# Optimization experiments

Hardware: AMD Instinct MI355X
Metric: run time of the kernel (lower is better)

Reference implementation:

```python
import jax, jax.numpy as jnp
import numpy as np

B, S, D, H = 2, 2048, 1024, 16
HD = D // H  # head_dim = 64


def setup_inputs() -> dict:
    key = jax.random.key(0)
    ks = jax.random.split(key, 11)
    sc = 1.0 / np.sqrt(D)
    inp = {
        "query": jax.random.normal(ks[0], (B, S, D), jnp.float32),
        "key_": jax.random.normal(ks[1], (B, S, D), jnp.float32),
        "value": jax.random.normal(ks[2], (B, S, D), jnp.float32),
        "Wq": jax.random.normal(ks[3], (D, D), jnp.float32) * sc,
        "bq": jnp.zeros((D,), jnp.float32),
        "Wk": jax.random.normal(ks[4], (D, D), jnp.float32) * sc,
        "bk": jnp.zeros((D,), jnp.float32),
        "Wv": jax.random.normal(ks[5], (D, D), jnp.float32) * sc,
        "bv": jnp.zeros((D,), jnp.float32),
        "Wo": jax.random.normal(ks[6], (D, D), jnp.float32) * sc,
        "bo": jnp.zeros((D,), jnp.float32),
    }
    return inp


def _split_heads(x):
    # [B,S,D] -> [B,H,S,HD]
    return x.reshape(B, -1, H, HD).transpose(0, 2, 1, 3)


def reference(query, key_, value, Wq, bq, Wk, bk, Wv, bv, Wo, bo):
    q = _split_heads(query @ Wq.T + bq)
    k = _split_heads(key_ @ Wk.T + bk)
    v = _split_heads(value @ Wv.T + bv)
    scores = jnp.einsum("bhqd,bhkd->bhqk", q, k) / jnp.sqrt(jnp.float32(HD))
    attn = jax.nn.softmax(scores, axis=-1)  # dropout is identity in eval
    out = jnp.einsum("bhqk,bhkd->bhqd", attn, v)
    out = out.transpose(0, 2, 1, 3).reshape(B, -1, D)
    return out @ Wo.T + bo
```

## Files before the change

### kernel.cpp

```cpp
#include <hip/hip_runtime.h>
#include <hip/hip_bf16.h>
#include <stdint.h>

#define B_  2
#define S_  2048
#define D_  1024
#define H_  16
#define HD_ 64
#define M_  (B_*S_)

typedef __bf16 bf16x8 __attribute__((ext_vector_type(8)));
typedef float  f32x4  __attribute__((ext_vector_type(4)));
typedef unsigned int u32x4 __attribute__((ext_vector_type(4)));
typedef unsigned int u32x2 __attribute__((ext_vector_type(2)));
typedef unsigned short ushort_t;
typedef ushort_t u16x8 __attribute__((ext_vector_type(8)));

#define LOG2E 1.44269504088896f

#if __has_builtin(__builtin_amdgcn_exp2f)
#define EXP2(x) __builtin_amdgcn_exp2f(x)
#else
#define EXP2(x) exp2f(x)
#endif

__device__ __forceinline__ ushort_t f2bf(float f) {
    return __builtin_bit_cast(ushort_t, (__bf16)f);
}
__device__ __forceinline__ bf16x8 load_frag(const ushort_t* p) {
    u32x4 r = *reinterpret_cast<const u32x4*>(p);
    return __builtin_bit_cast(bf16x8, r);
}
__device__ __forceinline__ bf16x8 lds_frag(const ushort_t* p) {
    u32x4 r = *reinterpret_cast<const u32x4*>(p);
    return __builtin_bit_cast(bf16x8, r);
}
__device__ __forceinline__ void gld_lds16(const ushort_t* g, ushort_t* l) {
    __builtin_amdgcn_global_load_lds(
        (const __attribute__((address_space(1))) void*)g,
        (__attribute__((address_space(3))) void*)l, 16, 0, 0);
}

__device__ __forceinline__ void cvt_body(const float* __restrict__ in,
                                         ushort_t* __restrict__ out, int i) {
    f32x4 v0 = *reinterpret_cast<const f32x4*>(in + i);
    f32x4 v1 = *reinterpret_cast<const f32x4*>(in + i + 4);
    u16x8 o;
#pragma unroll
    for (int j = 0; j < 4; ++j) { o[j] = f2bf(v0[j]); o[4 + j] = f2bf(v1[j]); }
    *reinterpret_cast<u16x8*>(out + i) = o;
}

__global__ __launch_bounds__(256) void cvt_all_kernel(
    const float* q, const float* k, const float* v,
    const float* fwq, const float* fwk, const float* fwv, const float* fwo,
    ushort_t* oq, ushort_t* ok, ushort_t* ov,
    ushort_t* owq, ushort_t* owk, ushort_t* owv, ushort_t* owo)
{
    const size_t T = (size_t)M_ * D_;
    const size_t U = (size_t)D_ * D_;
    const size_t idx = ((size_t)blockIdx.x * 256 + threadIdx.x) * 8;
    const float* in; ushort_t* out; size_t off;
    if (idx < 3 * T) {
        const size_t w = idx >> 22; off = idx & (T - 1);
        in  = (w == 0) ? q  : (w == 1) ? k  : v;
        out = (w == 0) ? oq : (w == 1) ? ok : ov;
    } else {
        const size_t r = idx - 3 * T;
        const size_t w = r >> 20; off = r & (U - 1);
        in  = (w == 0) ? fwq : (w == 1) ? fwk : (w == 2) ? fwv : fwo;
        out = (w == 0) ? owq : (w == 1) ? owk : (w == 2) ? owv : owo;
    }
    cvt_body(in, out, (int)off);
}

__device__ __forceinline__ void gemm_body(const ushort_t* __restrict__ X,
                                          const ushort_t* __restrict__ W,
                                          const float* __restrict__ bias,
                                          void* __restrict__ out, int mode)
{
    __shared__ ushort_t lA[2][128 * 32];
    __shared__ ushort_t lB[2][128 * 32];

    const int tid  = threadIdx.x;
    const int lane = tid & 63;
    const int wv   = tid >> 6;
    const int m0   = blockIdx.x * 128;
    const int n0   = blockIdx.y * 128;
    const int wr   = (wv >> 1) * 64;
    const int wc   = (wv & 1) * 64;
    const int l15  = lane & 15;
    const int lg   = lane >> 4;

    f32x4 acc[4][4];
#pragma unroll
    for (int i = 0; i < 4; ++i)
#pragma unroll
        for (int j = 0; j < 4; ++j) acc[i][j] = (f32x4){0.f, 0.f, 0.f, 0.f};

    const int srow = lane >> 2;
    const int sk   = (lane & 3) * 8;
    const int c0   = wv * 2, c1 = wv * 2 + 1;
    const size_t arow0 = (size_t)(m0 + c0 * 16 + srow) * D_ + sk;
    const size_t arow1 = (size_t)(m0 + c1 * 16 + srow) * D_ + sk;
    const size_t brow0 = (size_t)(n0 + c0 * 16 + srow) * D_ + sk;
    const size_t brow1 = (size_t)(n0 + c1 * 16 + srow) * D_ + sk;

    gld_lds16(X + arow0, &lA[0][c0 * 512]);
    gld_lds16(X + arow1, &lA[0][c1 * 512]);
    gld_lds16(W + brow0, &lB[0][c0 * 512]);
    gld_lds16(W + brow1, &lB[0][c1 * 512]);

    const int NKT = D_ / 32;
    for (int kt = 0; kt < NKT; ++kt) {
        const int cur = kt & 1;
        __builtin_amdgcn_s_barrier();
        if (kt + 1 < NKT) {
            const int k0 = (kt + 1) * 32;
            gld_lds16(X + arow0 + k0, &lA[cur ^ 1][c0 * 512]);
            gld_lds16(X + arow1 + k0, &lA[cur ^ 1][c1 * 512]);
            gld_lds16(W + brow0 + k0, &lB[cur ^ 1][c0 * 512]);
            gld_lds16(W + brow1 + k0, &lB[cur ^ 1][c1 * 512]);
            asm volatile("s_waitcnt vmcnt(4)" ::: "memory");
        } else {
            asm volatile("s_waitcnt vmcnt(0)" ::: "memory");
        }
        __builtin_amdgcn_s_barrier();

        bf16x8 a[4], b[4];
#pragma unroll
        for (int i = 0; i < 4; ++i)
            a[i] = lds_frag(&lA[cur][(wr + i * 16 + l15) * 32 + lg * 8]);
#pragma unroll
        for (int j = 0; j < 4; ++j)
            b[j] = lds_frag(&lB[cur][(wc + j * 16 + l15) * 32 + lg * 8]);
#pragma unroll
        for (int i = 0; i < 4; ++i)
#pragma unroll
            for (int j = 0; j < 4; ++j)
                acc[i][j] = __builtin_amdgcn_mfma_f32_16x16x32_bf16(a[i], b[j], acc[i][j], 0, 0, 0);
    }

#pragma unroll
    for (int i = 0; i < 4; ++i) {
#pragma unroll
        for (int j = 0; j < 4; ++j) {
            const int gcol = n0 + wc + j * 16 + l15;
            const float bv = bias[gcol];
#pragma unroll
            for (int r = 0; r < 4; ++r) {
                const int grow = m0 + wr + i * 16 + lg * 4 + r;
                float v = acc[i][j][r] + bv;
                if (mode == 0) v *= 0.125f * LOG2E;
                if (mode == 3) {
                    ((float*)out)[(size_t)grow * D_ + gcol] = v;
                } else {
                    const int b = grow >> 11, s = grow & (S_ - 1);
                    const int h = gcol >> 6,  hd = gcol & 63;
                    size_t addr;
                    if (mode == 2) addr = ((size_t)(b * H_ + h) * HD_ + hd) * S_ + s;
                    else           addr = ((size_t)(b * H_ + h) * S_ + s) * HD_ + hd;
                    ((ushort_t*)out)[addr] = f2bf(v);
                }
            }
        }
    }
}

__global__ __launch_bounds__(256) void qkv_kernel(
    const ushort_t* q_in, const ushort_t* k_in, const ushort_t* v_in,
    const ushort_t* Wq, const ushort_t* Wk, const ushort_t* Wv,
    const float* bq, const float* bk, const float* bv,
    ushort_t* qo, ushort_t* ko, ushort_t* vo)
{
    const int z = blockIdx.z;
    const ushort_t* X  = (z == 0) ? q_in : (z == 1) ? k_in : v_in;
    const ushort_t* W  = (z == 0) ? Wq   : (z == 1) ? Wk   : Wv;
    const float*    bs = (z == 0) ? bq   : (z == 1) ? bk   : bv;
    ushort_t*       o  = (z == 0) ? qo   : (z == 1) ? ko   : vo;
    gemm_body(X, W, bs, o, (z == 2) ? 2 : z);
}

__global__ __launch_bounds__(256) void oproj_kernel(
    const ushort_t* X, const ushort_t* W, const float* bias, float* out)
{
    gemm_body(X, W, bias, out, 3);
}

#define PSTRIDE 72
#define KVB 64
#define NT  (S_ / KVB)
#define AW  8

__global__ __launch_bounds__(512, 4) void attn_kernel(
    const ushort_t* __restrict__ Q, const ushort_t* __restrict__ K,
    const ushort_t* __restrict__ VT, ushort_t* __restrict__ O)
{
    __shared__ ushort_t kbuf[2][KVB * 64];
    __shared__ ushort_t vbuf[2][KVB * 64];
    __shared__ ushort_t plds[AW * 16 * PSTRIDE];

    const int lane  = threadIdx.x & 63;
    const int wv    = threadIdx.x >> 6;
    const int bh    = blockIdx.x;
    const int qb    = blockIdx.y;
    const int qbase = qb * (16 * AW) + wv * 16;
    const int l15   = lane & 15;
    const int lg    = lane >> 4;

    const ushort_t* Qp = Q  + (size_t)bh * S_ * HD_;
    const ushort_t* Kp = K  + (size_t)bh * S_ * HD_;
    const ushort_t* Vp = VT + (size_t)bh * HD_ * S_;

    const int st_id   = threadIdx.x & 255;
    const bool st_k   = (threadIdx.x < 256);
    const ushort_t* Sg = st_k ? Kp : Vp;
    const int gstride  = st_k ? HD_ : S_;
    const int gtile    = st_k ? (KVB * HD_) : KVB;

    const int sm0   = st_id;
    const int srow0 = sm0 >> 3;
    const int scb0  = ((sm0 & 7) ^ (srow0 & 7)) * 8;
    const int sm1   = 256 + st_id;
    const int srow1 = sm1 >> 3;
    const int scb1  = ((sm1 & 7) ^ (srow1 & 7)) * 8;

    int off[4][2];
#pragma unroll
    for (int x = 0; x < 4; ++x)
#pragma unroll
        for (int c = 0; c < 2; ++c)
            off[x][c] = (x * 16 + l15) * 64 + ((c * 32 + lg * 8) ^ ((l15 & 7) << 3));

    bf16x8 aq[2];
#pragma unroll
    for (int c = 0; c < 2; ++c)
        aq[c] = load_frag(Qp + (size_t)(qbase + l15) * HD_ + c * 32 + lg * 8);

    f32x4 accO[4];
#pragma unroll
    for (int dt = 0; dt < 4; ++dt) accO[dt] = (f32x4){0.f, 0.f, 0.f, 0.f};
    float lrun = 0.f;

    ushort_t* pbuf = &plds[wv * 16 * PSTRIDE];

    {
        ushort_t* dst = st_k ? kbuf[0] : vbuf[0];
        gld_lds16(Sg + (size_t)srow0 * gstride + scb0, dst + sm0 * 8);
        gld_lds16(Sg + (size_t)srow1 * gstride + scb1, dst + sm1 * 8);
    }

    for (int t = 0; t < NT; ++t) {
        const int cur = t & 1;
        const ushort_t* kb = kbuf[cur];
        const ushort_t* vb = vbuf[cur];

        __builtin_amdgcn_s_barrier();
        if (t + 1 < NT) {
            const ushort_t* g = Sg + (size_t)(t + 1) * gtile;
            ushort_t* dst = st_k ? kbuf[cur ^ 1] : vbuf[cur ^ 1];
            gld_lds16(g + (size_t)srow0 * gstride + scb0, dst + sm0 * 8);
            gld_lds16(g + (size_t)srow1 * gstride + scb1, dst + sm1 * 8);
            asm volatile("s_waitcnt vmcnt(2)" ::: "memory");
        } else {
            asm volatile("s_waitcnt vmcnt(0)" ::: "memory");
        }
        __builtin_amdgcn_s_barrier();

        f32x4 st[4];
#pragma unroll
        for (int j = 0; j < 4; ++j) st[j] = (f32x4){0.f, 0.f, 0.f, 0.f};
        __builtin_amdgcn_s_setprio(1);
#pragma unroll
        for (int j = 0; j < 4; ++j)
#pragma unroll
            for (int c = 0; c < 2; ++c)
                st[j] = __builtin_amdgcn_mfma_f32_16x16x32_bf16(
                    lds_frag(&kb[off[j][c]]), aq[c], st[j], 0, 0, 0);
        __builtin_amdgcn_s_setprio(0);

        float p[4][4];
#pragma unroll
        for (int j = 0; j < 4; ++j)
#pragma unroll
            for (int r = 0; r < 4; ++r)
                p[j][r] = EXP2(st[j][r]);

#pragma unroll
        for (int j = 0; j < 4; ++j) {
            u32x2 w;
            w[0] = (unsigned)f2bf(p[j][0]) | ((unsigned)f2bf(p[j][1]) << 16);
            w[1] = (unsigned)f2bf(p[j][2]) | ((unsigned)f2bf(p[j][3]) << 16);
            *reinterpret_cast<u32x2*>(&pbuf[l15 * PSTRIDE + j * 16 + lg * 4]) = w;
        }

        float s0 = (p[0][0] + p[0][1]) + (p[0][2] + p[0][3]);
        float s1 = (p[1][0] + p[1][1]) + (p[1][2] + p[1][3]);
        float s2 = (p[2][0] + p[2][1]) + (p[2][2] + p[2][3]);
        float s3 = (p[3][0] + p[3][1]) + (p[3][2] + p[3][3]);
        lrun += (s0 + s1) + (s2 + s3);

        bf16x8 ap[2];
#pragma unroll
        for (int c = 0; c < 2; ++c)
            ap[c] = lds_frag(&pbuf[l15 * PSTRIDE + c * 32 + lg * 8]);

        __builtin_amdgcn_s_setprio(1);
#pragma unroll
        for (int dt = 0; dt < 4; ++dt)
#pragma unroll
            for (int c = 0; c < 2; ++c)
                accO[dt] = __builtin_amdgcn_mfma_f32_16x16x32_bf16(
                    lds_frag(&vb[off[dt][c]]), ap[c], accO[dt], 0, 0, 0);
        __builtin_amdgcn_s_setprio(0);
    }

    lrun += __shfl_xor(lrun, 16);
    lrun += __shfl_xor(lrun, 32);
    const float inv = 1.0f / lrun;
    const int b = bh >> 4, h = bh & 15;
    const size_t rowbase = (size_t)(b * S_ + qbase + l15) * D_ + h * 64;
#pragma unroll
    for (int dt = 0; dt < 4; ++dt) {
        u32x2 w;
        w[0] = (unsigned)f2bf(accO[dt][0] * inv) | ((unsigned)f2bf(accO[dt][1] * inv) << 16);
        w[1] = (unsigned)f2bf(accO[dt][2] * inv) | ((unsigned)f2bf(accO[dt][3] * inv) << 16);
        *reinterpret_cast<u32x2*>(&O[rowbase + dt * 16 + lg * 4]) = w;
    }
}

extern "C" void kernel_launch(void* const* d_in, const int* in_sizes, int n_in,
                              void* d_out, int out_size, void* d_ws, size_t ws_size,
                              hipStream_t stream)
{
    const float* query = (const float*)d_in[0];
    const float* key_  = (const float*)d_in[1];
    const float* value = (const float*)d_in[2];
    const float* Wq    = (const float*)d_in[3];
    const float* bq    = (const float*)d_in[4];
    const float* Wk    = (const float*)d_in[5];
    const float* bk    = (const float*)d_in[6];
    const float* Wv    = (const float*)d_in[7];
    const float* bv    = (const float*)d_in[8];
    const float* Wo    = (const float*)d_in[9];
    const float* bo    = (const float*)d_in[10];

    ushort_t* ws   = (ushort_t*)d_ws;
    const size_t T = (size_t)M_ * D_;
    const size_t U = (size_t)D_ * D_;
    ushort_t* xq  = ws;
    ushort_t* xk  = xq + T;
    ushort_t* xv  = xk + T;
    ushort_t* wq  = xv + T;
    ushort_t* wk  = wq + U;
    ushort_t* wv  = wk + U;
    ushort_t* wo  = wv + U;
    ushort_t* qws  = wo + U;
    ushort_t* kws  = qws + T;
    ushort_t* vtws = kws + T;
    ushort_t* aows = vtws + T;

    const int cvt_blocks = (int)((3 * T + 4 * U) / (256 * 8));
    cvt_all_kernel<<<cvt_blocks, 256, 0, stream>>>(
        query, key_, value, Wq, Wk, Wv, Wo,
        xq, xk, xv, wq, wk, wv, wo);

    qkv_kernel<<<dim3(32, 8, 3), 256, 0, stream>>>(
        xq, xk, xv, wq, wk, wv, bq, bk, bv, qws, kws, vtws);

    attn_kernel<<<dim3(32, 16), 512, 0, stream>>>(qws, kws, vtws, aows);

    oproj_kernel<<<dim3(32, 8, 1), 256, 0, stream>>>(
        aows, wo, bo, (float*)d_out);
}
```

Measured before the change: 137.1 us.

## Triple-buffer GEMM K-loop and give each attention wave two query tiles

The projection GEMMs move from double to triple buffering of LDS tiles, prefetching two k-tiles ahead, with adjusted waitcnts and a scheduling barrier. The attention kernel drops from 8 waves of 16 query rows to 4 waves of 32 rows each. Every K/V fragment read from LDS is now reused by two MFMAs, halving LDS reads per FLOP. Costs are more registers and LDS per block, fewer waves for latency hiding, and the softmax (exp2, sum) skipping max subtraction as before.

Measured after the change: 129.0 us. 1.06x faster.

```diff
diff --git a/kernel.cpp b/kernel.cpp
--- a/kernel.cpp
+++ b/kernel.cpp
@@ -79,8 +79,8 @@
                                           const float* __restrict__ bias,
                                           void* __restrict__ out, int mode)
 {
-    __shared__ ushort_t lA[2][128 * 32];
-    __shared__ ushort_t lB[2][128 * 32];
+    __shared__ ushort_t lA[3][128 * 32];
+    __shared__ ushort_t lB[3][128 * 32];
 
     const int tid  = threadIdx.x;
     const int lane = tid & 63;
@@ -106,26 +106,32 @@
     const size_t brow0 = (size_t)(n0 + c0 * 16 + srow) * D_ + sk;
     const size_t brow1 = (size_t)(n0 + c1 * 16 + srow) * D_ + sk;
 
-    gld_lds16(X + arow0, &lA[0][c0 * 512]);
-    gld_lds16(X + arow1, &lA[0][c1 * 512]);
-    gld_lds16(W + brow0, &lB[0][c0 * 512]);
-    gld_lds16(W + brow1, &lB[0][c1 * 512]);
+    auto stage = [&](int ktile, int bufi) {
+        const int k0 = ktile * 32;
+        gld_lds16(X + arow0 + k0, &lA[bufi][c0 * 512]);
+        gld_lds16(X + arow1 + k0, &lA[bufi][c1 * 512]);
+        gld_lds16(W + brow0 + k0, &lB[bufi][c0 * 512]);
+        gld_lds16(W + brow1 + k0, &lB[bufi][c1 * 512]);
+    };
 
     const int NKT = D_ / 32;
+    stage(0, 0);
+    stage(1, 1);
+
+    int cur = 0;
     for (int kt = 0; kt < NKT; ++kt) {
-        const int cur = kt & 1;
         __builtin_amdgcn_s_barrier();
-        if (kt + 1 < NKT) {
-            const int k0 = (kt + 1) * 32;
-            gld_lds16(X + arow0 + k0, &lA[cur ^ 1][c0 * 512]);
-            gld_lds16(X + arow1 + k0, &lA[cur ^ 1][c1 * 512]);
-            gld_lds16(W + brow0 + k0, &lB[cur ^ 1][c0 * 512]);
-            gld_lds16(W + brow1 + k0, &lB[cur ^ 1][c1 * 512]);
+        if (kt + 2 < NKT) {
+            int nxt = cur + 2; if (nxt >= 3) nxt -= 3;
+            stage(kt + 2, nxt);
+            asm volatile("s_waitcnt vmcnt(8)" ::: "memory");
+        } else if (kt + 2 == NKT) {
             asm volatile("s_waitcnt vmcnt(4)" ::: "memory");
         } else {
             asm volatile("s_waitcnt vmcnt(0)" ::: "memory");
         }
         __builtin_amdgcn_s_barrier();
+        __builtin_amdgcn_sched_barrier(0);
 
         bf16x8 a[4], b[4];
 #pragma unroll
@@ -139,6 +145,8 @@
 #pragma unroll
             for (int j = 0; j < 4; ++j)
                 acc[i][j] = __builtin_amdgcn_mfma_f32_16x16x32_bf16(a[i], b[j], acc[i][j], 0, 0, 0);
+
+        cur = (cur == 2) ? 0 : cur + 1;
     }
 
 #pragma unroll
@@ -190,21 +198,20 @@
 #define PSTRIDE 72
 #define KVB 64
 #define NT  (S_ / KVB)
-#define AW  8
-
-__global__ __launch_bounds__(512, 4) void attn_kernel(
+
+__global__ __launch_bounds__(256, 2) void attn_kernel(
     const ushort_t* __restrict__ Q, const ushort_t* __restrict__ K,
     const ushort_t* __restrict__ VT, ushort_t* __restrict__ O)
 {
     __shared__ ushort_t kbuf[2][KVB * 64];
     __shared__ ushort_t vbuf[2][KVB * 64];
-    __shared__ ushort_t plds[AW * 16 * PSTRIDE];
+    __shared__ ushort_t plds[4 * 32 * PSTRIDE];
 
     const int lane  = threadIdx.x & 63;
     const int wv    = threadIdx.x >> 6;
     const int bh    = blockIdx.x;
     const int qb    = blockIdx.y;
-    const int qbase = qb * (16 * AW) + wv * 16;
+    const int qbase = qb * 128 + wv * 32;
     const int l15   = lane & 15;
     const int lg    = lane >> 4;
 
@@ -212,18 +219,19 @@
     const ushort_t* Kp = K  + (size_t)bh * S_ * HD_;
     const ushort_t* Vp = VT + (size_t)bh * HD_ * S_;
 
-    const int st_id   = threadIdx.x & 255;
-    const bool st_k   = (threadIdx.x < 256);
-    const ushort_t* Sg = st_k ? Kp : Vp;
-    const int gstride  = st_k ? HD_ : S_;
-    const int gtile    = st_k ? (KVB * HD_) : KVB;
-
-    const int sm0   = st_id;
-    const int srow0 = sm0 >> 3;
-    const int scb0  = ((sm0 & 7) ^ (srow0 & 7)) * 8;
-    const int sm1   = 256 + st_id;
-    const int srow1 = sm1 >> 3;
-    const int scb1  = ((sm1 & 7) ^ (srow1 & 7)) * 8;
+    const int mk0 = threadIdx.x;
+    const int mk1 = threadIdx.x + 256;
+    const int kr0 = mk0 >> 3, kc0 = ((mk0 & 7) ^ (kr0 & 7)) * 8;
+    const int kr1 = mk1 >> 3, kc1 = ((mk1 & 7) ^ (kr1 & 7)) * 8;
+
+    auto stage = [&](int tile, int bufi) {
+        const ushort_t* gK = Kp + (size_t)tile * KVB * HD_;
+        const ushort_t* gV = Vp + (size_t)tile * KVB;
+        gld_lds16(gK + (size_t)kr0 * HD_ + kc0, kbuf[bufi] + mk0 * 8);
+        gld_lds16(gK + (size_t)kr1 * HD_ + kc1, kbuf[bufi] + mk1 * 8);
+        gld_lds16(gV + (size_t)kr0 * S_  + kc0, vbuf[bufi] + mk0 * 8);
+        gld_lds16(gV + (size_t)kr1 * S_  + kc1, vbuf[bufi] + mk1 * 8);
+    };
 
     int off[4][2];
 #pragma unroll
@@ -232,23 +240,23 @@
         for (int c = 0; c < 2; ++c)
             off[x][c] = (x * 16 + l15) * 64 + ((c * 32 + lg * 8) ^ ((l15 & 7) << 3));
 
-    bf16x8 aq[2];
-#pragma unroll
-    for (int c = 0; c < 2; ++c)
-        aq[c] = load_frag(Qp + (size_t)(qbase + l15) * HD_ + c * 32 + lg * 8);
-
-    f32x4 accO[4];
-#pragma unroll
-    for (int dt = 0; dt < 4; ++dt) accO[dt] = (f32x4){0.f, 0.f, 0.f, 0.f};
-    float lrun = 0.f;
-
-    ushort_t* pbuf = &plds[wv * 16 * PSTRIDE];
-
-    {
-        ushort_t* dst = st_k ? kbuf[0] : vbuf[0];
-        gld_lds16(Sg + (size_t)srow0 * gstride + scb0, dst + sm0 * 8);
-        gld_lds16(Sg + (size_t)srow1 * gstride + scb1, dst + sm1 * 8);
-    }
+    bf16x8 aq[2][2];
+#pragma unroll
+    for (int qh = 0; qh < 2; ++qh)
+#pragma unroll
+        for (int c = 0; c < 2; ++c)
+            aq[c][qh] = load_frag(Qp + (size_t)(qbase + qh * 16 + l15) * HD_ + c * 32 + lg * 8);
+
+    f32x4 accO[4][2];
+#pragma unroll
+    for (int dt = 0; dt < 4; ++dt)
+#pragma unroll
+        for (int qh = 0; qh < 2; ++qh) accO[dt][qh] = (f32x4){0.f, 0.f, 0.f, 0.f};
+    float lrun0 = 0.f, lrun1 = 0.f;
+
+    ushort_t* pbuf = &plds[wv * 32 * PSTRIDE];
+
+    stage(0, 0);
 
     for (int t = 0; t < NT; ++t) {
         const int cur = t & 1;
@@ -257,75 +265,94 @@
 
         __builtin_amdgcn_s_barrier();
         if (t + 1 < NT) {
-            const ushort_t* g = Sg + (size_t)(t + 1) * gtile;
-            ushort_t* dst = st_k ? kbuf[cur ^ 1] : vbuf[cur ^ 1];
-            gld_lds16(g + (size_t)srow0 * gstride + scb0, dst + sm0 * 8);
-            gld_lds16(g + (size_t)srow1 * gstride + scb1, dst + sm1 * 8);
-            asm volatile("s_waitcnt vmcnt(2)" ::: "memory");
+            stage(t + 1, cur ^ 1);
+            asm volatile("s_waitcnt vmcnt(4)" ::: "memory");
         } else {
             asm volatile("s_waitcnt vmcnt(0)" ::: "memory");
         }
         __builtin_amdgcn_s_barrier();
-
-        f32x4 st[4];
-#pragma unroll
-        for (int j = 0; j < 4; ++j) st[j] = (f32x4){0.f, 0.f, 0.f, 0.f};
+        __builtin_amdgcn_sched_barrier(0);
+
+        f32x4 st[4][2];
+#pragma unroll
+        for (int j = 0; j < 4; ++j)
+#pragma unroll
+            for (int qh = 0; qh < 2; ++qh) st[j][qh] = (f32x4){0.f, 0.f, 0.f, 0.f};
         __builtin_amdgcn_s_setprio(1);
 #pragma unroll
-        for (int j = 0; j < 4; ++j)
+        for (int j = 0; j < 4; ++j) {
+            bf16x8 k0 = lds_frag(&kb[off[j][0]]);
+            bf16x8 k1 = lds_frag(&kb[off[j][1]]);
+            st[j][0] = __builtin_amdgcn_mfma_f32_16x16x32_bf16(k0, aq[0][0], st[j][0], 0, 0, 0);
+            st[j][0] = __builtin_amdgcn_mfma_f32_16x16x32_bf16(k1, aq[1][0], st[j][0], 0, 0, 0);
+            st[j][1] = __builtin_amdgcn_mfma_f32_16x16x32_bf16(k0, aq[0][1], st[j][1], 0, 0, 0);
+            st[j][1] = __builtin_amdgcn_mfma_f32_16x16x32_bf16(k1, aq[1][1], st[j][1], 0, 0, 0);
+        }
+        __builtin_amdgcn_s_setprio(0);
+
+#pragma unroll
+        for (int qh = 0; qh < 2; ++qh) {
+            float p[4][4];
+#pragma unroll
+            for (int j = 0; j < 4; ++j)
+#pragma unroll
+                for (int r = 0; r < 4; ++r)
+                    p[j][r] = EXP2(st[j][qh][r]);
+#pragma unroll
+            for (int j = 0; j < 4; ++j) {
+                u32x2 w;
+                w[0] = (unsigned)f2bf(p[j][0]) | ((unsigned)f2bf(p[j][1]) << 16);
+                w[1] = (unsigned)f2bf(p[j][2]) | ((unsigned)f2bf(p[j][3]) << 16);
+                *reinterpret_cast<u32x2*>(
+                    &pbuf[(qh * 16 + l15) * PSTRIDE + j * 16 + lg * 4]) = w;
+            }
+            float s0 = (p[0][0] + p[0][1]) + (p[0][2] + p[0][3]);
+            float s1 = (p[1][0] + p[1][1]) + (p[1][2] + p[1][3]);
+            float s2 = (p[2][0] + p[2][1]) + (p[2][2] + p[2][3]);
+            float s3 = (p[3][0] + p[3][1]) + (p[3][2] + p[3][3]);
+            if (qh == 0) lrun0 += (s0 + s1) + (s2 + s3);
+            else         lrun1 += (s0 + s1) + (s2 + s3);
+        }
+
+        bf16x8 ap[2][2];
+#pragma unroll
+        for (int qh = 0; qh < 2; ++qh)
 #pragma unroll
             for (int c = 0; c < 2; ++c)
-                st[j] = __builtin_amdgcn_mfma_f32_16x16x32_bf16(
-                    lds_frag(&kb[off[j][c]]), aq[c], st[j], 0, 0, 0);
-        __builtin_amdgcn_s_setprio(0);
-
-        float p[4][4];
-#pragma unroll
-        for (int j = 0; j < 4; ++j)
-#pragma unroll
-            for (int r = 0; r < 4; ++r)
-                p[j][r] = EXP2(st[j][r]);
-
-#pragma unroll
-        for (int j = 0; j < 4; ++j) {
-            u32x2 w;
-            w[0] = (unsigned)f2bf(p[j][0]) | ((unsigned)f2bf(p[j][1]) << 16);
-            w[1] = (unsigned)f2bf(p[j][2]) | ((unsigned)f2bf(p[j][3]) << 16);
-            *reinterpret_cast<u32x2*>(&pbuf[l15 * PSTRIDE + j * 16 + lg * 4]) = w;
-        }
-
-        float s0 = (p[0][0] + p[0][1]) + (p[0][2] + p[0][3]);
-        float s1 = (p[1][0] + p[1][1]) + (p[1][2] + p[1][3]);
-        float s2 = (p[2][0] + p[2][1]) + (p[2][2] + p[2][3]);
-        float s3 = (p[3][0] + p[3][1]) + (p[3][2] + p[3][3]);
-        lrun += (s0 + s1) + (s2 + s3);
-
-        bf16x8 ap[2];
-#pragma unroll
-        for (int c = 0; c < 2; ++c)
-            ap[c] = lds_frag(&pbuf[l15 * PSTRIDE + c * 32 + lg * 8]);
+                ap[c][qh] = lds_frag(&pbuf[(qh * 16 + l15) * PSTRIDE + c * 32 + lg * 8]);
 
         __builtin_amdgcn_s_setprio(1);
 #pragma unroll
-        for (int dt = 0; dt < 4; ++dt)
-#pragma unroll
-            for (int c = 0; c < 2; ++c)
-                accO[dt] = __builtin_amdgcn_mfma_f32_16x16x32_bf16(
-                    lds_frag(&vb[off[dt][c]]), ap[c], accO[dt], 0, 0, 0);
+        for (int dt = 0; dt < 4; ++dt) {
+            bf16x8 v0 = lds_frag(&vb[off[dt][0]]);
+            bf16x8 v1 = lds_frag(&vb[off[dt][1]]);
+            accO[dt][0] = __builtin_amdgcn_mfma_f32_16x16x32_bf16(v0, ap[0][0], accO[dt][0], 0, 0, 0);
+            accO[dt][0] = __builtin_amdgcn_mfma_f32_16x16x32_bf16(v1, ap[1][0], accO[dt][0], 0, 0, 0);
+            accO[dt][1] = __builtin_amdgcn_mfma_f32_16x16x32_bf16(v0, ap[0][1], accO[dt][1], 0, 0, 0);
+            accO[dt][1] = __builtin_amdgcn_mfma_f32_16x16x32_bf16(v1, ap[1][1], accO[dt][1], 0, 0, 0);
+        }
         __builtin_amdgcn_s_setprio(0);
     }
 
-    lrun += __shfl_xor(lrun, 16);
-    lrun += __shfl_xor(lrun, 32);
-    const float inv = 1.0f / lrun;
+    lrun0 += __shfl_xor(lrun0, 16);
+    lrun0 += __shfl_xor(lrun0, 32);
+    lrun1 += __shfl_xor(lrun1, 16);
+    lrun1 += __shfl_xor(lrun1, 32);
     const int b = bh >> 4, h = bh & 15;
-    const size_t rowbase = (size_t)(b * S_ + qbase + l15) * D_ + h * 64;
-#pragma unroll
-    for (int dt = 0; dt < 4; ++dt) {
-        u32x2 w;
-        w[0] = (unsigned)f2bf(accO[dt][0] * inv) | ((unsigned)f2bf(accO[dt][1] * inv) << 16);
-        w[1] = (unsigned)f2bf(accO[dt][2] * inv) | ((unsigned)f2bf(accO[dt][3] * inv) << 16);
-        *reinterpret_cast<u32x2*>(&O[rowbase + dt * 16 + lg * 4]) = w;
+#pragma unroll
+    for (int qh = 0; qh < 2; ++qh) {
+        const float inv = 1.0f / (qh == 0 ? lrun0 : lrun1);
+        const size_t rowbase =
+            (size_t)(b * S_ + qbase + qh * 16 + l15) * D_ + h * 64;
+#pragma unroll
+        for (int dt = 0; dt < 4; ++dt) {
+            u32x2 w;
+            w[0] = (unsigned)f2bf(accO[dt][qh][0] * inv) |
+                   ((unsigned)f2bf(accO[dt][qh][1] * inv) << 16);
+            w[1] = (unsigned)f2bf(accO[dt][qh][2] * inv) |
+                   ((unsigned)f2bf(accO[dt][qh][3] * inv) << 16);
+            *reinterpret_cast<u32x2*>(&O[rowbase + dt * 16 + lg * 4]) = w;
+        }
     }
 }
 
@@ -368,7 +395,7 @@
     qkv_kernel<<<dim3(32, 8, 3), 256, 0, stream>>>(
         xq, xk, xv, wq, wk, wv, bq, bk, bv, qws, kws, vtws);
 
-    attn_kernel<<<dim3(32, 16), 512, 0, stream>>>(qws, kws, vtws, aows);
+    attn_kernel<<<dim3(32, 16), 256, 0, stream>>>(qws, kws, vtws, aows);
 
     oproj_kernel<<<dim3(32, 8, 1), 256, 0, stream>>>(
         aows, wo, bo, (float*)d_out);
```
